# Kernel optimization log

Hardware: AMD Instinct MI355X
Metric: run time of the kernel (lower is better)

## Reference

```python
import jax, jax.numpy as jnp
import numpy as np

PATCH_SIZE = 64
NUM_PATCHES = 32
PRUNE_RATE = 0.1


def setup_inputs() -> dict:
    key = jax.random.key(0)
    k1, k2, k3, k4 = jax.random.split(key, 4)
    B, L, H, E = 8, 1024, 8, 64
    queries = jax.random.normal(k1, (B, L, H, E), dtype=jnp.float32)
    keys = jax.random.normal(k2, (B, L, H, E), dtype=jnp.float32)
    values = jax.random.normal(k3, (B, L, H, E), dtype=jnp.float32)
    # random.randint(0, L - patch_size) is inclusive -> maxval = L - patch_size + 1
    starts = jax.random.randint(k4, (NUM_PATCHES,), 0, L - PATCH_SIZE + 1, dtype=jnp.int32)
    return {"queries": queries, "keys": keys, "values": values, "starts": starts}


def _patch_mask(starts, L):
    # in_patch[p, i] = start_p <= i < start_p + PATCH_SIZE
    idx = jnp.arange(L)
    in_patch = (idx[None, :] >= starts[:, None]) & (idx[None, :] < starts[:, None] + PATCH_SIZE)
    f = in_patch.astype(jnp.float32)
    # union over patches of outer-product block masks -> [L, L]
    return jnp.einsum('pi,pj->ij', f, f) > 0


def reference(queries, keys, values, starts):
    B, L, H, E = queries.shape
    mask = _patch_mask(starts, L)                              # [L, L]
    # dense per-head dot products; zero outside the patch blocks (as torch fills)
    scores = jnp.einsum('blhe,bshe->bhls', queries, keys)      # [B, H, L, L]
    scores = jnp.where(mask[None, None], scores, jnp.float32(0.0))
    abs_scores = jnp.abs(scores)
    # torch.quantile default 'linear' interpolation == jnp.quantile default
    threshold = jnp.quantile(abs_scores, PRUNE_RATE, axis=-1, keepdims=True)
    scores = jnp.where(abs_scores < threshold, -jnp.inf, scores)
    A = jax.nn.softmax(scores, axis=-1)                        # dropout p=0.0 -> identity
    V = jnp.einsum('bhls,bshd->blhd', A, values)               # [B, L, H, D]
    return V
```

## Files before the change

kernel.cpp:

```cpp
#include <hip/hip_runtime.h>

#define LQ 1024
#define NP 32
#define CC 2.0611536224385579e-9f

typedef __attribute__((ext_vector_type(8))) short short8v;
typedef __attribute__((ext_vector_type(4))) float f32x4;

__device__ __forceinline__ unsigned short bf16hi(float f) {
  unsigned u = __float_as_uint(f);
  u += 0x7fffu + ((u >> 16) & 1u);
  return (unsigned short)(u >> 16);
}
__device__ __forceinline__ float bf16tof(unsigned short b) {
  return __uint_as_float(((unsigned)b) << 16);
}
__device__ __forceinline__ void gload16(const unsigned short* g, unsigned short* l) {
  __builtin_amdgcn_global_load_lds(
      (const __attribute__((address_space(1))) unsigned int*)g,
      (__attribute__((address_space(3))) unsigned int*)l, 16, 0, 0);
}
#define SWZD(d) (((d) & 7) ^ ((d) >> 3))

__global__ __launch_bounds__(256) void prep_kernel(const float* __restrict__ K,
                                                   const float* __restrict__ V,
                                                   unsigned short* __restrict__ planes,
                                                   float* __restrict__ partial) {
  __shared__ unsigned short Vt[4096];
  __shared__ float red[16][64];
  const int blk = blockIdx.x;
  const int sc = blk & 15, h = (blk >> 4) & 7, b = blk >> 7;
  const int tid = threadIdx.x;
  unsigned short* pb = planes + (size_t)blk * 12288;
  const float* Kb = K + ((size_t)b * LQ + sc * 64) * 512 + h * 64;
  const float* Vb = V + ((size_t)b * LQ + sc * 64) * 512 + h * 64;
  const int c4 = tid & 15;
  float facc[4] = {0.f, 0.f, 0.f, 0.f};
#pragma unroll
  for (int t = 0; t < 4; ++t) {
    const int sr = t * 16 + (tid >> 4);
    const float4 kv = *(const float4*)(Kb + (size_t)sr * 512 + c4 * 4);
    ushort4 h4, l4;
    {
      float fv[4] = {kv.x, kv.y, kv.z, kv.w};
#pragma unroll
      for (int i = 0; i < 4; ++i) {
        unsigned short hb = bf16hi(fv[i]);
        ((unsigned short*)&h4)[i] = hb;
        ((unsigned short*)&l4)[i] = bf16hi(fv[i] - bf16tof(hb));
      }
    }
    const int kidx = sr * 64 + (((c4 >> 1) ^ (sr & 7)) * 8) + (c4 & 1) * 4;
    *(ushort4*)&pb[kidx] = h4;
    *(ushort4*)&pb[4096 + kidx] = l4;
    const float4 vv = *(const float4*)(Vb + (size_t)sr * 512 + c4 * 4);
    {
      float fv[4] = {vv.x, vv.y, vv.z, vv.w};
#pragma unroll
      for (int i = 0; i < 4; ++i) {
        facc[i] += fv[i];
        const int d = c4 * 4 + i;
        Vt[d * 64 + (((sr >> 3) ^ SWZD(d)) * 8) + (sr & 7)] = bf16hi(fv[i]);
      }
    }
  }
#pragma unroll
  for (int i = 0; i < 4; ++i) red[tid >> 4][c4 * 4 + i] = facc[i];
  __syncthreads();
  if (tid < 64) {
    float s = 0.f;
#pragma unroll
    for (int g = 0; g < 16; ++g) s += red[g][tid];
    partial[(size_t)blk * 64 + tid] = s;
  }
#pragma unroll
  for (int it = 0; it < 2; ++it) {
    const int idx = (it * 256 + tid) * 8;
    *(uint4*)&pb[8192 + idx] = *(const uint4*)&Vt[idx];
  }
}

__global__ __launch_bounds__(256) void attn_kernel(const float* __restrict__ Q,
                                                   const unsigned short* __restrict__ planes,
                                                   const int* __restrict__ starts,
                                                   const float* __restrict__ partial,
                                                   float* __restrict__ out) {
  __shared__ unsigned short ldsb[2][12288];
  __shared__ unsigned short Plds[4096];
  __shared__ int lotab[64], hitab[64];

  const int tid = threadIdx.x;
  const int lane = tid & 63;
  const int w = tid >> 6;
  const int lr = lane & 15, lg = lane >> 4;
  const int blk = ((blockIdx.x & 7) << 7) | (blockIdx.x >> 3);
  const int grp = blk & 15, bh = blk >> 4;
  const int h = bh & 7, b = bh >> 3;
  const int L0 = grp << 6;
  int w0 = L0 - 64; w0 = w0 < 0 ? 0 : (w0 > LQ - 192 ? LQ - 192 : w0);

  if (tid < 64) {
    int row = L0 + tid, lo = 0x7fffffff, hi = 0;
#pragma unroll
    for (int p = 0; p < NP; ++p) {
      int sp = starts[p];
      if ((unsigned)(row - sp) < 64u) { lo = min(lo, sp); hi = max(hi, sp + 64); }
    }
    lotab[tid] = lo; hitab[tid] = hi;
  }
  int lo_l = 0x7fffffff, hi_l = 0;
  {
    int row = L0 + lane;
#pragma unroll
    for (int p = 0; p < NP; ++p) {
      int sp = starts[p];
      if ((unsigned)(row - sp) < 64u) { lo_l = min(lo_l, sp); hi_l = max(hi_l, sp + 64); }
    }
  }
  int rlo = lo_l, rhi = hi_l;
#pragma unroll
  for (int off = 32; off; off >>= 1) {
    rlo = min(rlo, __shfl_xor(rlo, off));
    rhi = max(rhi, __shfl_xor(rhi, off));
  }
  rlo = __builtin_amdgcn_readfirstlane(rlo);
  rhi = __builtin_amdgcn_readfirstlane(rhi);

  int csl[3], ncs = 0;
#pragma unroll
  for (int c = 0; c < 3; ++c) {
    const int cs = w0 + c * 64;
    if (cs < rhi && cs + 64 > rlo) csl[ncs++] = cs;
  }

  const unsigned short* gpb = planes + (size_t)bh * 16 * 12288;
  auto stage = [&](int cs, int buf) {
    const unsigned short* gp = gpb + (size_t)(cs >> 6) * 12288 + w * 3072 + lane * 8;
    unsigned short* lp = &ldsb[buf][w * 3072];
#pragma unroll
    for (int k = 0; k < 6; ++k) gload16(gp + k * 512, lp + k * 512);
  };

  if (ncs) stage(csl[0], 0);

  const float* Qrow = Q + ((size_t)b * LQ + L0 + w * 16 + lr) * 512 + h * 64;
  short8v qhi[2], qlo[2];
#pragma unroll
  for (int ks = 0; ks < 2; ++ks) {
    float4 a = *(const float4*)(Qrow + ks * 32 + lg * 8);
    float4 c = *(const float4*)(Qrow + ks * 32 + lg * 8 + 4);
    short8v hi8, lo8;
    float fv[8] = {a.x, a.y, a.z, a.w, c.x, c.y, c.z, c.w};
#pragma unroll
    for (int i = 0; i < 8; ++i) {
      unsigned short hb = bf16hi(fv[i]);
      hi8[i] = (short)hb;
      lo8[i] = (short)bf16hi(fv[i] - bf16tof(hb));
    }
    qhi[ks] = hi8; qlo[ks] = lo8;
  }

  __syncthreads();

  int lo_r[4], hi_r[4];
#pragma unroll
  for (int r = 0; r < 4; ++r) {
    lo_r[r] = lotab[w * 16 + lg * 4 + r];
    hi_r[r] = hitab[w * 16 + lg * 4 + r];
  }

  f32x4 oacc[4];
  float zloc[4] = {0.f, 0.f, 0.f, 0.f};
#pragma unroll
  for (int n = 0; n < 4; ++n) oacc[n] = (f32x4){0.f, 0.f, 0.f, 0.f};

  for (int i = 0; i < ncs; ++i) {
    if (i + 1 < ncs) stage(csl[i + 1], (i + 1) & 1);
    const unsigned short* Khi_l = &ldsb[i & 1][0];
    const unsigned short* Klo_l = &ldsb[i & 1][4096];
    const unsigned short* Vt_l  = &ldsb[i & 1][8192];
    const int cs = csl[i];

    f32x4 sacc[4];
#pragma unroll
    for (int n = 0; n < 4; ++n) sacc[n] = (f32x4){0.f, 0.f, 0.f, 0.f};

#pragma unroll
    for (int ks = 0; ks < 2; ++ks) {
#pragma unroll
      for (int n = 0; n < 4; ++n) {
        const int srow = n * 16 + lr;
        const int idx = srow * 64 + (((ks * 4 + lg) ^ (srow & 7)) * 8);
        const short8v kbh = *(const short8v*)&Khi_l[idx];
        const short8v kbl = *(const short8v*)&Klo_l[idx];
        sacc[n] = __builtin_amdgcn_mfma_f32_16x16x32_bf16(qhi[ks], kbh, sacc[n], 0, 0, 0);
        sacc[n] = __builtin_amdgcn_mfma_f32_16x16x32_bf16(qhi[ks], kbl, sacc[n], 0, 0, 0);
        sacc[n] = __builtin_amdgcn_mfma_f32_16x16x32_bf16(qlo[ks], kbh, sacc[n], 0, 0, 0);
      }
    }

#pragma unroll
    for (int n = 0; n < 4; ++n) {
#pragma unroll
      for (int r = 0; r < 4; ++r) {
        const int sg = cs + n * 16 + lr;
        float p = 0.f;
        if (sg >= lo_r[r] && sg < hi_r[r]) p = __expf(sacc[n][r] - 20.f) - CC;
        const unsigned short pb16 = bf16hi(p);
        zloc[r] += bf16tof(pb16);
        const int prow = w * 16 + lg * 4 + r;
        const int sl = n * 16 + lr;
        Plds[prow * 64 + (((sl >> 3) ^ ((prow & 7) ^ (prow >> 3))) * 8) + (sl & 7)] = pb16;
      }
    }

#pragma unroll
    for (int ks = 0; ks < 2; ++ks) {
      const int prow = w * 16 + lr;
      const short8v pa = *(const short8v*)
          &Plds[prow * 64 + (((ks * 4 + lg) ^ ((prow & 7) ^ (prow >> 3))) * 8)];
#pragma unroll
      for (int n = 0; n < 4; ++n) {
        const int d = n * 16 + lr;
        const short8v vb = *(const short8v*)&Vt_l[d * 64 + (((ks * 4 + lg) ^ SWZD(d)) * 8)];
        oacc[n] = __builtin_amdgcn_mfma_f32_16x16x32_bf16(pa, vb, oacc[n], 0, 0, 0);
      }
    }
    __syncthreads();
  }

#pragma unroll
  for (int r = 0; r < 4; ++r) {
#pragma unroll
    for (int off = 1; off < 16; off <<= 1) zloc[r] += __shfl_xor(zloc[r], off, 64);
  }

  float sv[4];
#pragma unroll
  for (int n = 0; n < 4; ++n) {
    float s = 0.f;
#pragma unroll
    for (int sc2 = 0; sc2 < 16; ++sc2)
      s += partial[(size_t)bh * 1024 + sc2 * 64 + n * 16 + lr];
    sv[n] = s;
  }

  float* Ob = out + ((size_t)b * LQ + L0 + w * 16 + lg * 4) * 512 + h * 64;
#pragma unroll
  for (int r = 0; r < 4; ++r) {
    const float invz = 1.f / (zloc[r] + 1024.f * CC);
#pragma unroll
    for (int n = 0; n < 4; ++n)
      Ob[(size_t)r * 512 + n * 16 + lr] = (oacc[n][r] + CC * sv[n]) * invz;
  }
}

extern "C" void kernel_launch(void* const* d_in, const int* in_sizes, int n_in,
                              void* d_out, int out_size, void* d_ws, size_t ws_size,
                              hipStream_t stream) {
  const float* Q      = (const float*)d_in[0];
  const float* K      = (const float*)d_in[1];
  const float* V      = (const float*)d_in[2];
  const int*   starts = (const int*)d_in[3];
  float* out = (float*)d_out;
  unsigned short* planes = (unsigned short*)d_ws;
  float* partial = (float*)((char*)d_ws + 25165824);

  prep_kernel<<<1024, 256, 0, stream>>>(K, V, planes, partial);
  attn_kernel<<<1024, 256, 0, stream>>>(Q, planes, starts, partial, out);
}
```

Measured before the change: 114.3 us.

## Fuse K/V bf16 split conversion into attention kernel, drop precomputed planes

The prep kernel no longer writes hi/lo bf16 K planes and transposed bf16 V to workspace. It only computes column sums of V. The attention kernel now loads fp32 K/V tiles into registers, converts and swizzles them into a single LDS buffer, and prefetches the next tile into registers while the current one is computed. This removes the planes round-trip through global memory and shrinks LDS use, at the cost of repeated per-block conversion of overlapping K/V tiles, register-staged rather than async LDS loads, and extra barriers per iteration.

```diff
diff --git a/kernel.cpp b/kernel.cpp
--- a/kernel.cpp
+++ b/kernel.cpp
@@ -15,57 +15,24 @@
 __device__ __forceinline__ float bf16tof(unsigned short b) {
   return __uint_as_float(((unsigned)b) << 16);
 }
-__device__ __forceinline__ void gload16(const unsigned short* g, unsigned short* l) {
-  __builtin_amdgcn_global_load_lds(
-      (const __attribute__((address_space(1))) unsigned int*)g,
-      (__attribute__((address_space(3))) unsigned int*)l, 16, 0, 0);
-}
 #define SWZD(d) (((d) & 7) ^ ((d) >> 3))
 
-__global__ __launch_bounds__(256) void prep_kernel(const float* __restrict__ K,
-                                                   const float* __restrict__ V,
-                                                   unsigned short* __restrict__ planes,
+__global__ __launch_bounds__(256) void sumv_kernel(const float* __restrict__ V,
                                                    float* __restrict__ partial) {
-  __shared__ unsigned short Vt[4096];
   __shared__ float red[16][64];
   const int blk = blockIdx.x;
   const int sc = blk & 15, h = (blk >> 4) & 7, b = blk >> 7;
   const int tid = threadIdx.x;
-  unsigned short* pb = planes + (size_t)blk * 12288;
-  const float* Kb = K + ((size_t)b * LQ + sc * 64) * 512 + h * 64;
+  const int c4 = tid & 15;
   const float* Vb = V + ((size_t)b * LQ + sc * 64) * 512 + h * 64;
-  const int c4 = tid & 15;
-  float facc[4] = {0.f, 0.f, 0.f, 0.f};
+  float4 facc = make_float4(0.f, 0.f, 0.f, 0.f);
 #pragma unroll
   for (int t = 0; t < 4; ++t) {
     const int sr = t * 16 + (tid >> 4);
-    const float4 kv = *(const float4*)(Kb + (size_t)sr * 512 + c4 * 4);
-    ushort4 h4, l4;
-    {
-      float fv[4] = {kv.x, kv.y, kv.z, kv.w};
-#pragma unroll
-      for (int i = 0; i < 4; ++i) {
-        unsigned short hb = bf16hi(fv[i]);
-        ((unsigned short*)&h4)[i] = hb;
-        ((unsigned short*)&l4)[i] = bf16hi(fv[i] - bf16tof(hb));
-      }
-    }
-    const int kidx = sr * 64 + (((c4 >> 1) ^ (sr & 7)) * 8) + (c4 & 1) * 4;
-    *(ushort4*)&pb[kidx] = h4;
-    *(ushort4*)&pb[4096 + kidx] = l4;
-    const float4 vv = *(const float4*)(Vb + (size_t)sr * 512 + c4 * 4);
-    {
-      float fv[4] = {vv.x, vv.y, vv.z, vv.w};
-#pragma unroll
-      for (int i = 0; i < 4; ++i) {
-        facc[i] += fv[i];
-        const int d = c4 * 4 + i;
-        Vt[d * 64 + (((sr >> 3) ^ SWZD(d)) * 8) + (sr & 7)] = bf16hi(fv[i]);
-      }
-    }
-  }
-#pragma unroll
-  for (int i = 0; i < 4; ++i) red[tid >> 4][c4 * 4 + i] = facc[i];
+    const float4 v = *(const float4*)(Vb + (size_t)sr * 512 + c4 * 4);
+    facc.x += v.x; facc.y += v.y; facc.z += v.z; facc.w += v.w;
+  }
+  *(float4*)&red[tid >> 4][c4 * 4] = facc;
   __syncthreads();
   if (tid < 64) {
     float s = 0.f;
@@ -73,20 +40,15 @@
     for (int g = 0; g < 16; ++g) s += red[g][tid];
     partial[(size_t)blk * 64 + tid] = s;
   }
-#pragma unroll
-  for (int it = 0; it < 2; ++it) {
-    const int idx = (it * 256 + tid) * 8;
-    *(uint4*)&pb[8192 + idx] = *(const uint4*)&Vt[idx];
-  }
 }
 
 __global__ __launch_bounds__(256) void attn_kernel(const float* __restrict__ Q,
-                                                   const unsigned short* __restrict__ planes,
+                                                   const float* __restrict__ K,
+                                                   const float* __restrict__ V,
                                                    const int* __restrict__ starts,
                                                    const float* __restrict__ partial,
                                                    float* __restrict__ out) {
-  __shared__ unsigned short ldsb[2][12288];
-  __shared__ unsigned short Plds[4096];
+  __shared__ unsigned short Kh[4096], Kl[4096], Vt[4096], Plds[4096];
   __shared__ int lotab[64], hitab[64];
 
   const int tid = threadIdx.x;
@@ -99,6 +61,9 @@
   const int L0 = grp << 6;
   int w0 = L0 - 64; w0 = w0 < 0 ? 0 : (w0 > LQ - 192 ? LQ - 192 : w0);
 
+  const float* Kb = K + (size_t)b * LQ * 512 + h * 64;
+  const float* Vb = V + (size_t)b * LQ * 512 + h * 64;
+
   if (tid < 64) {
     int row = L0 + tid, lo = 0x7fffffff, hi = 0;
 #pragma unroll
@@ -133,15 +98,41 @@
     if (cs < rhi && cs + 64 > rlo) csl[ncs++] = cs;
   }
 
-  const unsigned short* gpb = planes + (size_t)bh * 16 * 12288;
-  auto stage = [&](int cs, int buf) {
-    const unsigned short* gp = gpb + (size_t)(cs >> 6) * 12288 + w * 3072 + lane * 8;
-    unsigned short* lp = &ldsb[buf][w * 3072];
-#pragma unroll
-    for (int k = 0; k < 6; ++k) gload16(gp + k * 512, lp + k * 512);
+  float4 kreg[4], vreg[4];
+  const int c4 = tid & 15;
+  auto gload = [&](int cs) {
+#pragma unroll
+    for (int t = 0; t < 4; ++t) {
+      const int sr = t * 16 + (tid >> 4);
+      kreg[t] = *(const float4*)(Kb + (size_t)(cs + sr) * 512 + c4 * 4);
+      vreg[t] = *(const float4*)(Vb + (size_t)(cs + sr) * 512 + c4 * 4);
+    }
   };
-
-  if (ncs) stage(csl[0], 0);
+  auto lwrite = [&]() {
+#pragma unroll
+    for (int t = 0; t < 4; ++t) {
+      const int sr = t * 16 + (tid >> 4);
+      ushort4 h4, l4;
+      float fk[4] = {kreg[t].x, kreg[t].y, kreg[t].z, kreg[t].w};
+#pragma unroll
+      for (int i = 0; i < 4; ++i) {
+        unsigned short hb = bf16hi(fk[i]);
+        ((unsigned short*)&h4)[i] = hb;
+        ((unsigned short*)&l4)[i] = bf16hi(fk[i] - bf16tof(hb));
+      }
+      const int kidx = sr * 64 + (((c4 >> 1) ^ (sr & 7)) * 8) + (c4 & 1) * 4;
+      *(ushort4*)&Kh[kidx] = h4;
+      *(ushort4*)&Kl[kidx] = l4;
+      float fv[4] = {vreg[t].x, vreg[t].y, vreg[t].z, vreg[t].w};
+#pragma unroll
+      for (int i = 0; i < 4; ++i) {
+        const int d = c4 * 4 + i;
+        Vt[d * 64 + (((sr >> 3) ^ SWZD(d)) * 8) + (sr & 7)] = bf16hi(fv[i]);
+      }
+    }
+  };
+
+  if (ncs) gload(csl[0]);
 
   const float* Qrow = Q + ((size_t)b * LQ + L0 + w * 16 + lr) * 512 + h * 64;
   short8v qhi[2], qlo[2];
@@ -160,6 +151,10 @@
     qhi[ks] = hi8; qlo[ks] = lo8;
   }
 
+  if (ncs) {
+    lwrite();
+    if (ncs > 1) gload(csl[1]);
+  }
   __syncthreads();
 
   int lo_r[4], hi_r[4];
@@ -175,12 +170,7 @@
   for (int n = 0; n < 4; ++n) oacc[n] = (f32x4){0.f, 0.f, 0.f, 0.f};
 
   for (int i = 0; i < ncs; ++i) {
-    if (i + 1 < ncs) stage(csl[i + 1], (i + 1) & 1);
-    const unsigned short* Khi_l = &ldsb[i & 1][0];
-    const unsigned short* Klo_l = &ldsb[i & 1][4096];
-    const unsigned short* Vt_l  = &ldsb[i & 1][8192];
     const int cs = csl[i];
-
     f32x4 sacc[4];
 #pragma unroll
     for (int n = 0; n < 4; ++n) sacc[n] = (f32x4){0.f, 0.f, 0.f, 0.f};
@@ -191,8 +181,8 @@
       for (int n = 0; n < 4; ++n) {
         const int srow = n * 16 + lr;
         const int idx = srow * 64 + (((ks * 4 + lg) ^ (srow & 7)) * 8);
-        const short8v kbh = *(const short8v*)&Khi_l[idx];
-        const short8v kbl = *(const short8v*)&Klo_l[idx];
+        const short8v kbh = *(const short8v*)&Kh[idx];
+        const short8v kbl = *(const short8v*)&Kl[idx];
         sacc[n] = __builtin_amdgcn_mfma_f32_16x16x32_bf16(qhi[ks], kbh, sacc[n], 0, 0, 0);
         sacc[n] = __builtin_amdgcn_mfma_f32_16x16x32_bf16(qhi[ks], kbl, sacc[n], 0, 0, 0);
         sacc[n] = __builtin_amdgcn_mfma_f32_16x16x32_bf16(qlo[ks], kbh, sacc[n], 0, 0, 0);
@@ -222,11 +212,17 @@
 #pragma unroll
       for (int n = 0; n < 4; ++n) {
         const int d = n * 16 + lr;
-        const short8v vb = *(const short8v*)&Vt_l[d * 64 + (((ks * 4 + lg) ^ SWZD(d)) * 8)];
+        const short8v vb = *(const short8v*)&Vt[d * 64 + (((ks * 4 + lg) ^ SWZD(d)) * 8)];
         oacc[n] = __builtin_amdgcn_mfma_f32_16x16x32_bf16(pa, vb, oacc[n], 0, 0, 0);
       }
     }
-    __syncthreads();
+
+    if (i + 1 < ncs) {
+      __syncthreads();
+      lwrite();
+      if (i + 2 < ncs) gload(csl[i + 2]);
+      __syncthreads();
+    }
   }
 
 #pragma unroll
@@ -262,10 +258,9 @@
   const float* K      = (const float*)d_in[1];
   const float* V      = (const float*)d_in[2];
   const int*   starts = (const int*)d_in[3];
-  float* out = (float*)d_out;
-  unsigned short* planes = (unsigned short*)d_ws;
-  float* partial = (float*)((char*)d_ws + 25165824);
-
-  prep_kernel<<<1024, 256, 0, stream>>>(K, V, planes, partial);
-  attn_kernel<<<1024, 256, 0, stream>>>(Q, planes, starts, partial, out);
-}
+  float* out     = (float*)d_out;
+  float* partial = (float*)d_ws;
+
+  sumv_kernel<<<1024, 256, 0, stream>>>(V, partial);
+  attn_kernel<<<1024, 256, 0, stream>>>(Q, K, V, starts, partial, out);
+}
```

Result: no change. 114.0 us (-0.3%).
